# Performance work log

Hardware: AMD Instinct MI355X
Metric: run time of the kernel (lower is better)

The kernel has to match this reference:

```python
import jax, jax.numpy as jnp
import numpy as np

NEG = -1e30  # log-space 'zero' (bf16/fp32 safe, avoids -inf NaN propagation)
EPS = 1e-7   # keras.backend.epsilon(), added before log as in ctc_batch_cost


def _lse3(a, b, c):
    # stable logsumexp over three stacked log-values
    m = jnp.maximum(jnp.maximum(a, b), c)
    return m + jnp.log(jnp.exp(a - m) + jnp.exp(b - m) + jnp.exp(c - m))


def setup_inputs() -> dict:
    key = jax.random.key(0)
    k1, k2 = jax.random.split(key)
    B, T, C, L = 256, 512, 1024, 64
    # y_pred must be softmax probabilities (ctc_batch_cost takes log(p + eps))
    y_pred = jax.nn.softmax(jax.random.normal(k1, (B, T, C), dtype=jnp.float32), axis=-1)
    # labels in [0, C-1): never equal to blank (= C-1); no -1 padding here,
    # so label_length = L for every row, matching the layer's mask computation
    y_true = jax.random.randint(k2, (B, L), 0, C - 1).astype(jnp.int32)
    return {"y_true": y_true, "y_pred": y_pred}


def reference(y_true, y_pred):
    B, T, C = y_pred.shape
    L = y_true.shape[1]
    blank = C - 1  # tf classic CTC: blank is the last class
    S = 2 * L + 1

    lp = jnp.log(y_pred + EPS)                      # [B, T, C]
    ll = jnp.sum(y_true != -1, axis=1)              # [B] label lengths (mask of -1)

    # extended label sequence: blank, l1, blank, l2, ..., blank
    labels = jnp.where(y_true < 0, blank, y_true)
    ext = jnp.full((B, S), blank, dtype=y_true.dtype).at[:, 1::2].set(labels)

    # emission log-probs gathered at extended-label classes: e[b,t,s] = lp[b,t,ext[b,s]]
    idx = jnp.broadcast_to(ext[:, None, :], (B, T, S))
    e = jnp.take_along_axis(lp, idx, axis=2)        # [B, T, S]

    pos = jnp.arange(S)
    valid = pos[None, :] < (2 * ll + 1)[:, None]    # states within this row's DP band
    # skip transition s-2 -> s allowed iff ext[s] != blank and ext[s] != ext[s-2]
    allow2 = jnp.zeros((B, S), bool).at[:, 2:].set(
        (ext[:, 2:] != blank) & (ext[:, 2:] != ext[:, :-2]))

    alpha0 = jnp.where((pos[None, :] < 2) & valid, e[:, 0, :], NEG)  # [B, S]
    neg_col = jnp.full((B, 1), NEG, dtype=lp.dtype)

    def step(alpha, e_t):
        p1 = jnp.concatenate([neg_col, alpha[:, :-1]], axis=1)
        p2 = jnp.concatenate([neg_col, neg_col, alpha[:, :-2]], axis=1)
        p2 = jnp.where(allow2, p2, NEG)
        new = jnp.where(valid, e_t + _lse3(alpha, p1, p2), NEG)
        return new, None

    # input_length = T for every row (as computed in the layer)
    alpha_T, _ = jax.lax.scan(step, alpha0, jnp.swapaxes(e, 0, 1)[1:])

    a_last = jnp.take_along_axis(alpha_T, (2 * ll)[:, None], axis=1)[:, 0]
    a_prev = jnp.take_along_axis(alpha_T, jnp.maximum(2 * ll - 1, 0)[:, None], axis=1)[:, 0]
    a_prev = jnp.where(ll > 0, a_prev, NEG)
    loss = -jnp.logaddexp(a_last, a_prev)           # [B]
    return loss[:, None]                            # ctc_batch_cost returns [B, 1]
```

## Files before the change

kernel.cpp:

```cpp
#include <hip/hip_runtime.h>


constexpr int B = 256, T = 512, C = 1024, L = 64;
constexpr int P = 8;
#define NEGV (-1e30f)
#define EPSV (1e-7f)
constexpr float LN2F = 0.69314718055994530942f;

__device__ __forceinline__ float fexp2(float x) { return __builtin_amdgcn_exp2f(x); }
__device__ __forceinline__ float flog2(float x) { return __builtin_amdgcn_logf(x); }

__global__ __launch_bounds__(64, 1)
void ctc_loss_kernel(const int* __restrict__ y_true,
                     const float* __restrict__ y_pred,
                     float* __restrict__ out) {
    const int b    = blockIdx.x;
    const int lane = threadIdx.x;
    const float* p = y_pred + (size_t)b * T * C;

    int lab = y_true[b * L + lane];
    int cls = (lab < 0) ? (C - 1) : lab;
    unsigned long long m = __ballot(lab != -1);
    int ll = __popcll(m);
    int clsprev = __shfl_up(cls, 1);
    const bool allow    = (lane > 0) && (cls != C - 1) && (cls != clsprev);
    const bool lblValid = (lane < ll);
    const bool blkValid = (lane <= ll);
    const bool b64Valid = (ll == 64);

    float eb0 = flog2(p[C - 1] + EPSV);
    float el0 = flog2(p[cls]   + EPSV);
    float bv  = (lane == 0)            ? eb0 : NEGV;
    float lv  = (lane == 0 && ll >= 1) ? el0 : NEGV;
    float b64 = NEGV;

    float bufL[P], bufB[P];
#pragma unroll
    for (int k = 0; k < P; ++k) {
        size_t off = (size_t)(1 + k) * C;
        bufL[k] = p[off + cls];
        bufB[k] = p[off + (C - 1)];
    }

    for (int t0 = 1; t0 < T; t0 += P) {
#pragma unroll
        for (int k = 0; k < P; ++k) {
            int t = t0 + k;
            if (t >= T) break;
            float vl = bufL[k];
            float vb = bufB[k];
            int tp = t + P; if (tp > T - 1) tp = T - 1;
            size_t off = (size_t)tp * C;
            bufL[k] = p[off + cls];
            bufB[k] = p[off + (C - 1)];

            float el = flog2(vl + EPSV);
            float eb = flog2(vb + EPSV);

            float lprev = __shfl_up(lv, 1);
            if (lane == 0) lprev = NEGV;

            float m1 = fmaxf(bv, lprev);
            float nb = m1 + flog2(fexp2(bv - m1) + fexp2(lprev - m1)) + eb;
            nb = blkValid ? nb : NEGV;

            float p2 = allow ? lprev : NEGV;
            float m2 = fmaxf(fmaxf(lv, bv), p2);
            float nl = m2 + flog2(fexp2(lv - m2) + fexp2(bv - m2) + fexp2(p2 - m2)) + el;
            nl = lblValid ? nl : NEGV;

            float m3 = fmaxf(b64, lv);
            float nb64 = m3 + flog2(fexp2(b64 - m3) + fexp2(lv - m3)) + eb;
            nb64 = b64Valid ? nb64 : NEGV;

            bv = nb; lv = nl; b64 = nb64;
        }
    }

    float a_last = (ll == 64) ? __shfl(b64, 63) : __shfl(bv, ll);
    float a_prev = (ll > 0)   ? __shfl(lv, ll - 1) : NEGV;
    if (lane == 0) {
        float mm = fmaxf(a_last, a_prev);
        float loss = -(LN2F * (mm + flog2(fexp2(a_last - mm) + fexp2(a_prev - mm))));
        out[b] = loss;
    }
}

extern "C" void kernel_launch(void* const* d_in, const int* in_sizes, int n_in,
                              void* d_out, int out_size, void* d_ws, size_t ws_size,
                              hipStream_t stream) {
    const int*   y_true = (const int*)d_in[0];
    const float* y_pred = (const float*)d_in[1];
    float*       out    = (float*)d_out;
    ctc_loss_kernel<<<B, 64, 0, stream>>>(y_true, y_pred, out);
}
```

Before: 699.0 us.

## Run CTC recursion in linear probability space with LDS-staged gathers

The forward recursion now works in linear probability space, using plain multiply-adds in place of log-sum-exp. Every 8 steps it applies a wave-wide power-of-two rescale and tracks the accumulated exponent so the values do not underflow. A 1024-thread block gathers the emission probabilities for 128 timesteps into LDS in parallel, then one wave runs the serial recursion from LDS. This removes the per-step transcendentals and the global-memory latency on the critical path. In exchange there are two block barriers per chunk, 15 waves sit idle during the recursion, and the change relies on the periodic rescale keeping values within fp32 range. It also drops the valid-band masking and relies on zero initial values instead.

Result: faster. 672.6 us (-3.8%).

```diff
diff --git a/kernel.cpp b/kernel.cpp
--- a/kernel.cpp
+++ b/kernel.cpp
@@ -2,87 +2,110 @@
 
 
 constexpr int B = 256, T = 512, C = 1024, L = 64;
-constexpr int P = 8;
-#define NEGV (-1e30f)
+constexpr int BLK   = 1024;
+constexpr int NW    = BLK / 64;
+constexpr int CHUNK = 128;
+constexpr int TPW   = CHUNK / NW;
+constexpr int STRIDE = 66;
 #define EPSV (1e-7f)
 constexpr float LN2F = 0.69314718055994530942f;
 
-__device__ __forceinline__ float fexp2(float x) { return __builtin_amdgcn_exp2f(x); }
 __device__ __forceinline__ float flog2(float x) { return __builtin_amdgcn_logf(x); }
 
-__global__ __launch_bounds__(64, 1)
+__global__ __launch_bounds__(BLK, 1)
 void ctc_loss_kernel(const int* __restrict__ y_true,
                      const float* __restrict__ y_pred,
                      float* __restrict__ out) {
+    __shared__ float e_lds[CHUNK * STRIDE];
+
     const int b    = blockIdx.x;
-    const int lane = threadIdx.x;
+    const int tid  = threadIdx.x;
+    const int lane = tid & 63;
+    const int wave = tid >> 6;
     const float* p = y_pred + (size_t)b * T * C;
 
     int lab = y_true[b * L + lane];
     int cls = (lab < 0) ? (C - 1) : lab;
-    unsigned long long m = __ballot(lab != -1);
-    int ll = __popcll(m);
+    unsigned long long msk = __ballot(lab != -1);
+    int ll = __popcll(msk);
     int clsprev = __shfl_up(cls, 1);
-    const bool allow    = (lane > 0) && (cls != C - 1) && (cls != clsprev);
-    const bool lblValid = (lane < ll);
-    const bool blkValid = (lane <= ll);
-    const bool b64Valid = (ll == 64);
+    const bool allow = (lane > 0) && (cls != C - 1) && (cls != clsprev);
 
-    float eb0 = flog2(p[C - 1] + EPSV);
-    float el0 = flog2(p[cls]   + EPSV);
-    float bv  = (lane == 0)            ? eb0 : NEGV;
-    float lv  = (lane == 0 && ll >= 1) ? el0 : NEGV;
-    float b64 = NEGV;
+    float bv = 0.f, lv = 0.f, b64 = 0.f;
+    float shift = 0.f;
 
-    float bufL[P], bufB[P];
+    for (int c = 0; c < T / CHUNK; ++c) {
+        const int tbase = c * CHUNK;
+
+        {
+            const int t0 = tbase + wave * TPW;
+            float r[TPW];
 #pragma unroll
-    for (int k = 0; k < P; ++k) {
-        size_t off = (size_t)(1 + k) * C;
-        bufL[k] = p[off + cls];
-        bufB[k] = p[off + (C - 1)];
+            for (int k = 0; k < TPW; ++k)
+                r[k] = p[(size_t)(t0 + k) * C + cls];
+            float vb = 0.f;
+            if (lane < TPW)
+                vb = p[(size_t)(t0 + lane) * C + (C - 1)];
+#pragma unroll
+            for (int k = 0; k < TPW; ++k)
+                e_lds[(t0 - tbase + k) * STRIDE + lane] = r[k] + EPSV;
+            if (lane < TPW)
+                e_lds[(t0 - tbase + lane) * STRIDE + 64] = vb + EPSV;
+        }
+        __syncthreads();
+
+        if (wave == 0) {
+            for (int g = 0; g < CHUNK; g += 8) {
+                float elr[8], ebr[8];
+#pragma unroll
+                for (int k = 0; k < 8; ++k) {
+                    elr[k] = e_lds[(g + k) * STRIDE + lane];
+                    ebr[k] = e_lds[(g + k) * STRIDE + 64];
+                }
+#pragma unroll
+                for (int k = 0; k < 8; ++k) {
+                    const int t = tbase + g + k;
+                    const float el = elr[k], eb = ebr[k];
+                    if (t == 0) {
+                        bv  = (lane == 0) ? eb : 0.f;
+                        lv  = (lane == 0 && ll >= 1) ? el : 0.f;
+                        b64 = 0.f;
+                    } else {
+                        float lprev = __shfl_up(lv, 1);
+                        if (lane == 0) lprev = 0.f;
+                        float nb   = (bv + lprev) * eb;
+                        float p2   = allow ? lprev : 0.f;
+                        float nl   = (lv + bv + p2) * el;
+                        float nb64 = (b64 + lv) * eb;
+                        bv = nb; lv = nl; b64 = nb64;
+                    }
+                    if ((t & 7) == 7) {
+                        float mx = fmaxf(fmaxf(bv, lv), b64);
+#pragma unroll
+                        for (int s = 1; s < 64; s <<= 1)
+                            mx = fmaxf(mx, __shfl_xor(mx, s));
+                        unsigned u = __float_as_uint(mx);
+                        int e = (int)((u >> 23) & 0xFF);
+                        int sb = 314 - e;
+                        if (sb > 254) sb = 254;
+                        if (sb < 1)   sb = 1;
+                        float scale = __uint_as_float((unsigned)sb << 23);
+                        bv *= scale; lv *= scale; b64 *= scale;
+                        shift += (float)(sb - 127);
+                    }
+                }
+            }
+        }
+        __syncthreads();
     }
 
-    for (int t0 = 1; t0 < T; t0 += P) {
-#pragma unroll
-        for (int k = 0; k < P; ++k) {
-            int t = t0 + k;
-            if (t >= T) break;
-            float vl = bufL[k];
-            float vb = bufB[k];
-            int tp = t + P; if (tp > T - 1) tp = T - 1;
-            size_t off = (size_t)tp * C;
-            bufL[k] = p[off + cls];
-            bufB[k] = p[off + (C - 1)];
-
-            float el = flog2(vl + EPSV);
-            float eb = flog2(vb + EPSV);
-
-            float lprev = __shfl_up(lv, 1);
-            if (lane == 0) lprev = NEGV;
-
-            float m1 = fmaxf(bv, lprev);
-            float nb = m1 + flog2(fexp2(bv - m1) + fexp2(lprev - m1)) + eb;
-            nb = blkValid ? nb : NEGV;
-
-            float p2 = allow ? lprev : NEGV;
-            float m2 = fmaxf(fmaxf(lv, bv), p2);
-            float nl = m2 + flog2(fexp2(lv - m2) + fexp2(bv - m2) + fexp2(p2 - m2)) + el;
-            nl = lblValid ? nl : NEGV;
-
-            float m3 = fmaxf(b64, lv);
-            float nb64 = m3 + flog2(fexp2(b64 - m3) + fexp2(lv - m3)) + eb;
-            nb64 = b64Valid ? nb64 : NEGV;
-
-            bv = nb; lv = nl; b64 = nb64;
+    if (wave == 0) {
+        float a_last = (ll == 64) ? __shfl(b64, 63) : __shfl(bv, ll);
+        float a_prev = (ll > 0)   ? __shfl(lv, ll - 1) : 0.f;
+        if (lane == 0) {
+            float s = a_last + a_prev;
+            out[b] = -(flog2(s) - shift) * LN2F;
         }
-    }
-
-    float a_last = (ll == 64) ? __shfl(b64, 63) : __shfl(bv, ll);
-    float a_prev = (ll > 0)   ? __shfl(lv, ll - 1) : NEGV;
-    if (lane == 0) {
-        float mm = fmaxf(a_last, a_prev);
-        float loss = -(LN2F * (mm + flog2(fexp2(a_last - mm) + fexp2(a_prev - mm))));
-        out[b] = loss;
     }
 }
 
@@ -92,5 +115,5 @@
     const int*   y_true = (const int*)d_in[0];
     const float* y_pred = (const float*)d_in[1];
     float*       out    = (float*)d_out;
-    ctc_loss_kernel<<<B, 64, 0, stream>>>(y_true, y_pred, out);
+    ctc_loss_kernel<<<B, BLK, 0, stream>>>(y_true, y_pred, out);
 }
```
